# Kernel tuning notes

Hardware: AMD Instinct MI355X
Metric: run time of the kernel (lower is better)

## Reference

```python
import jax, jax.numpy as jnp
import numpy as np


def _binarize(x):
    # tf.where(x < 0, -1.0, 1.0)
    return jnp.where(x < 0, -1.0, 1.0).astype(jnp.float32)


def setup_inputs() -> dict:
    key = jax.random.key(0)
    k1, k2, k3 = jax.random.split(key, 3)
    M, K, N = 8192, 2048, 2048
    inputs = jax.random.normal(k1, (M, K), dtype=jnp.float32)
    kernel = jax.random.normal(k2, (K, N), dtype=jnp.float32) * 0.1
    bias = jax.random.normal(k3, (N,), dtype=jnp.float32) * 0.01
    return {"inputs": inputs, "kernel": kernel, "bias": bias}


def reference(inputs, kernel, bias):
    bx = _binarize(inputs)          # [M, K] in {-1, +1}
    bw = _binarize(kernel)          # [K, N] in {-1, +1}
    return jnp.matmul(bx, bw) + bias  # [M, N]
```

## Files before the change

### kernel.cpp

```cpp
#include <hip/hip_runtime.h>
#include <stdint.h>

typedef __attribute__((ext_vector_type(4))) int int4v;
typedef __attribute__((ext_vector_type(16))) unsigned char uchar16;

#define MDIM 8192
#define KDIM 2048
#define NDIM 2048
#define BM 128
#define BN 128
#define BK 128

__device__ __forceinline__ void load16_lds(const void* g, void* l) {
  __builtin_amdgcn_global_load_lds(
      (const __attribute__((address_space(1))) void*)g,
      (__attribute__((address_space(3))) void*)l, 16, 0, 0);
}

#define XBLK 4096
#define WBLK 1024

__global__ void binarize_fused(const float* __restrict__ X,
                               const float* __restrict__ W,
                               unsigned char* __restrict__ Xb,
                               unsigned char* __restrict__ WbT) {
  const int b = blockIdx.x;
  if (b < XBLK) {
    size_t i = ((size_t)b * 256 + threadIdx.x) * 16;
    const float4* xp = (const float4*)(X + i);
    uchar16 o;
#pragma unroll
    for (int h = 0; h < 4; ++h) {
      float4 a = xp[h];
      o[4 * h + 0] = (a.x < 0.f) ? 0xFFu : 0x01u;
      o[4 * h + 1] = (a.y < 0.f) ? 0xFFu : 0x01u;
      o[4 * h + 2] = (a.z < 0.f) ? 0xFFu : 0x01u;
      o[4 * h + 3] = (a.w < 0.f) ? 0xFFu : 0x01u;
    }
    *(uchar16*)(Xb + i) = o;
  } else {
    const int bw = b - XBLK;
    const int nb = bw & 31;
    const int kb = bw >> 5;
    const int nn = threadIdx.x & 63;
    const int kc = kb * 4 + (threadIdx.x >> 6);
    const float* wp = W + (size_t)(kc * 16) * NDIM + nb * 64 + nn;
    uchar16 o;
#pragma unroll
    for (int j = 0; j < 16; ++j)
      o[j] = (wp[(size_t)j * NDIM] < 0.f) ? 0xFFu : 0x01u;
    *(uchar16*)(WbT + (size_t)(nb * 64 + nn) * KDIM + kc * 16) = o;
  }
}

__global__ __launch_bounds__(256) void gemm_bin_i8(
    const unsigned char* __restrict__ A,
    const unsigned char* __restrict__ B,
    const float* __restrict__ bias,
    float* __restrict__ C) {
  __shared__ __align__(16) unsigned char As[BM * BK];
  __shared__ __align__(16) unsigned char Bs[BN * BK];

  const int tid = threadIdx.x;
  const int lane = tid & 63;
  const int wv = tid >> 6;
  const int wm = wv >> 1;
  const int wn = wv & 1;
  const int r = lane & 15;
  const int q = lane >> 4;

  const int m0 = blockIdx.x * BM;
  const int n0 = blockIdx.y * BN;

  int4v acc[4][4] = {};

  const int qbase = wv * 256;

  int srcoff[4];
#pragma unroll
  for (int i = 0; i < 4; ++i) {
    const int s = qbase + i * 64 + lane;
    const int row = s >> 3;
    const int cg = (s & 7) ^ (row & 7);
    srcoff[i] = row * KDIM + cg * 16;
  }

  for (int kb = 0; kb < KDIM; kb += BK) {
#pragma unroll
    for (int i = 0; i < 4; ++i) {
      load16_lds(A + (size_t)m0 * KDIM + kb + srcoff[i],
                 As + (size_t)(qbase + i * 64) * 16);
      load16_lds(B + (size_t)n0 * KDIM + kb + srcoff[i],
                 Bs + (size_t)(qbase + i * 64) * 16);
    }
    __syncthreads();

#pragma unroll
    for (int s2 = 0; s2 < 2; ++s2) {
      const int cswz = ((s2 * 4 + q) ^ (r & 7)) * 16;
      int4v af[4], bf[4];
#pragma unroll
      for (int t = 0; t < 4; ++t) {
        af[t] = *(const int4v*)(As + (wm * 64 + t * 16 + r) * BK + cswz);
        bf[t] = *(const int4v*)(Bs + (wn * 64 + t * 16 + r) * BK + cswz);
      }
#pragma unroll
      for (int tm = 0; tm < 4; ++tm)
#pragma unroll
        for (int tn = 0; tn < 4; ++tn)
          acc[tm][tn] = __builtin_amdgcn_mfma_i32_16x16x64_i8(
              af[tm], bf[tn], acc[tm][tn], 0, 0, 0);
    }
    __syncthreads();
  }

#pragma unroll
  for (int tn = 0; tn < 4; ++tn) {
    const int col = n0 + wn * 64 + tn * 16 + r;
    const float bv = bias[col];
#pragma unroll
    for (int tm = 0; tm < 4; ++tm) {
      const int rowb = m0 + wm * 64 + tm * 16 + q * 4;
#pragma unroll
      for (int v = 0; v < 4; ++v)
        C[(size_t)(rowb + v) * NDIM + col] = (float)acc[tm][tn][v] + bv;
    }
  }
}

extern "C" void kernel_launch(void* const* d_in, const int* in_sizes, int n_in,
                              void* d_out, int out_size, void* d_ws, size_t ws_size,
                              hipStream_t stream) {
  const float* X = (const float*)d_in[0];
  const float* W = (const float*)d_in[1];
  const float* bias = (const float*)d_in[2];
  float* out = (float*)d_out;

  unsigned char* Xb = (unsigned char*)d_ws;
  unsigned char* WbT = Xb + (size_t)MDIM * KDIM;

  binarize_fused<<<dim3(XBLK + WBLK), 256, 0, stream>>>(X, W, Xb, WbT);
  gemm_bin_i8<<<dim3(MDIM / BM, NDIM / BN), 256, 0, stream>>>(Xb, WbT, bias, out);
}
```

Baseline: 167.9 us.

## Switch binary GEMM from int8 MFMA to packed FP4 scaled MFMA

Binarized values are now packed as FP4 nibbles (±1.0 encoded as 0x2/0xA), two per byte, instead of one int8 per element. The GEMM uses the 16x16x128 f8f6f4 scaled MFMA with FP4 operand types and unit scales, halving the bytes moved per K step and doubling K per instruction. This should cut global and LDS traffic and MFMA count. The FP4 operand only fills half of each 8-int register vector, and the remaining lanes are zero-padded. Float accumulation stays exact for sums of ±1 within this range.

```diff
diff --git a/kernel.cpp b/kernel.cpp
--- a/kernel.cpp
+++ b/kernel.cpp
@@ -2,6 +2,8 @@
 #include <stdint.h>
 
 typedef __attribute__((ext_vector_type(4))) int int4v;
+typedef __attribute__((ext_vector_type(8))) int int8v;
+typedef __attribute__((ext_vector_type(4))) float floatx4;
 typedef __attribute__((ext_vector_type(16))) unsigned char uchar16;
 
 #define MDIM 8192
@@ -9,7 +11,8 @@
 #define NDIM 2048
 #define BM 128
 #define BN 128
-#define BK 128
+#define KB 1024
+#define BKB 128
 
 __device__ __forceinline__ void load16_lds(const void* g, void* l) {
   __builtin_amdgcn_global_load_lds(
@@ -17,8 +20,8 @@
       (__attribute__((address_space(3))) void*)l, 16, 0, 0);
 }
 
-#define XBLK 4096
-#define WBLK 1024
+#define XBLK 2048
+#define WBLK 512
 
 __global__ void binarize_fused(const float* __restrict__ X,
                                const float* __restrict__ W,
@@ -26,40 +29,45 @@
                                unsigned char* __restrict__ WbT) {
   const int b = blockIdx.x;
   if (b < XBLK) {
-    size_t i = ((size_t)b * 256 + threadIdx.x) * 16;
+    size_t i = ((size_t)b * 256 + threadIdx.x) * 32;
     const float4* xp = (const float4*)(X + i);
     uchar16 o;
 #pragma unroll
-    for (int h = 0; h < 4; ++h) {
+    for (int h = 0; h < 8; ++h) {
       float4 a = xp[h];
-      o[4 * h + 0] = (a.x < 0.f) ? 0xFFu : 0x01u;
-      o[4 * h + 1] = (a.y < 0.f) ? 0xFFu : 0x01u;
-      o[4 * h + 2] = (a.z < 0.f) ? 0xFFu : 0x01u;
-      o[4 * h + 3] = (a.w < 0.f) ? 0xFFu : 0x01u;
+      unsigned n0 = (a.x < 0.f) ? 0xAu : 0x2u;
+      unsigned n1 = (a.y < 0.f) ? 0xAu : 0x2u;
+      unsigned n2 = (a.z < 0.f) ? 0xAu : 0x2u;
+      unsigned n3 = (a.w < 0.f) ? 0xAu : 0x2u;
+      o[2 * h]     = (unsigned char)(n0 | (n1 << 4));
+      o[2 * h + 1] = (unsigned char)(n2 | (n3 << 4));
     }
-    *(uchar16*)(Xb + i) = o;
+    *(uchar16*)(Xb + i / 2) = o;
   } else {
     const int bw = b - XBLK;
     const int nb = bw & 31;
     const int kb = bw >> 5;
     const int nn = threadIdx.x & 63;
     const int kc = kb * 4 + (threadIdx.x >> 6);
-    const float* wp = W + (size_t)(kc * 16) * NDIM + nb * 64 + nn;
+    const float* wp = W + (size_t)(kc * 32) * NDIM + nb * 64 + nn;
     uchar16 o;
 #pragma unroll
-    for (int j = 0; j < 16; ++j)
-      o[j] = (wp[(size_t)j * NDIM] < 0.f) ? 0xFFu : 0x01u;
-    *(uchar16*)(WbT + (size_t)(nb * 64 + nn) * KDIM + kc * 16) = o;
+    for (int j = 0; j < 16; ++j) {
+      unsigned lo = (wp[(size_t)(2 * j) * NDIM] < 0.f) ? 0xAu : 0x2u;
+      unsigned hi = (wp[(size_t)(2 * j + 1) * NDIM] < 0.f) ? 0xAu : 0x2u;
+      o[j] = (unsigned char)(lo | (hi << 4));
+    }
+    *(uchar16*)(WbT + (size_t)(nb * 64 + nn) * KB + kc * 16) = o;
   }
 }
 
-__global__ __launch_bounds__(256) void gemm_bin_i8(
+__global__ __launch_bounds__(256) void gemm_bin_fp4(
     const unsigned char* __restrict__ A,
     const unsigned char* __restrict__ B,
     const float* __restrict__ bias,
     float* __restrict__ C) {
-  __shared__ __align__(16) unsigned char As[BM * BK];
-  __shared__ __align__(16) unsigned char Bs[BN * BK];
+  __shared__ __align__(16) unsigned char As[BM * BKB];
+  __shared__ __align__(16) unsigned char Bs[BN * BKB];
 
   const int tid = threadIdx.x;
   const int lane = tid & 63;
@@ -72,7 +80,7 @@
   const int m0 = blockIdx.x * BM;
   const int n0 = blockIdx.y * BN;
 
-  int4v acc[4][4] = {};
+  floatx4 acc[4][4] = {};
 
   const int qbase = wv * 256;
 
@@ -82,15 +90,15 @@
     const int s = qbase + i * 64 + lane;
     const int row = s >> 3;
     const int cg = (s & 7) ^ (row & 7);
-    srcoff[i] = row * KDIM + cg * 16;
+    srcoff[i] = row * KB + cg * 16;
   }
 
-  for (int kb = 0; kb < KDIM; kb += BK) {
+  for (int kb = 0; kb < KB; kb += BKB) {
 #pragma unroll
     for (int i = 0; i < 4; ++i) {
-      load16_lds(A + (size_t)m0 * KDIM + kb + srcoff[i],
+      load16_lds(A + (size_t)m0 * KB + kb + srcoff[i],
                  As + (size_t)(qbase + i * 64) * 16);
-      load16_lds(B + (size_t)n0 * KDIM + kb + srcoff[i],
+      load16_lds(B + (size_t)n0 * KB + kb + srcoff[i],
                  Bs + (size_t)(qbase + i * 64) * 16);
     }
     __syncthreads();
@@ -98,18 +106,21 @@
 #pragma unroll
     for (int s2 = 0; s2 < 2; ++s2) {
       const int cswz = ((s2 * 4 + q) ^ (r & 7)) * 16;
-      int4v af[4], bf[4];
+      int8v a8[4], b8[4];
 #pragma unroll
       for (int t = 0; t < 4; ++t) {
-        af[t] = *(const int4v*)(As + (wm * 64 + t * 16 + r) * BK + cswz);
-        bf[t] = *(const int4v*)(Bs + (wn * 64 + t * 16 + r) * BK + cswz);
+        int4v av = *(const int4v*)(As + (wm * 64 + t * 16 + r) * BKB + cswz);
+        int4v bv = *(const int4v*)(Bs + (wn * 64 + t * 16 + r) * BKB + cswz);
+        a8[t] = int8v{av[0], av[1], av[2], av[3], 0, 0, 0, 0};
+        b8[t] = int8v{bv[0], bv[1], bv[2], bv[3], 0, 0, 0, 0};
       }
 #pragma unroll
       for (int tm = 0; tm < 4; ++tm)
 #pragma unroll
         for (int tn = 0; tn < 4; ++tn)
-          acc[tm][tn] = __builtin_amdgcn_mfma_i32_16x16x64_i8(
-              af[tm], bf[tn], acc[tm][tn], 0, 0, 0);
+          acc[tm][tn] = __builtin_amdgcn_mfma_scale_f32_16x16x128_f8f6f4(
+              a8[tm], b8[tn], acc[tm][tn], 4, 4,
+              0, 0x7F7F7F7F, 0, 0x7F7F7F7F);
     }
     __syncthreads();
   }
@@ -123,7 +134,7 @@
       const int rowb = m0 + wm * 64 + tm * 16 + q * 4;
 #pragma unroll
       for (int v = 0; v < 4; ++v)
-        C[(size_t)(rowb + v) * NDIM + col] = (float)acc[tm][tn][v] + bv;
+        C[(size_t)(rowb + v) * NDIM + col] = acc[tm][tn][v] + bv;
     }
   }
 }
@@ -137,8 +148,8 @@
   float* out = (float*)d_out;
 
   unsigned char* Xb = (unsigned char*)d_ws;
-  unsigned char* WbT = Xb + (size_t)MDIM * KDIM;
+  unsigned char* WbT = Xb + (size_t)MDIM * KDIM / 2;
 
   binarize_fused<<<dim3(XBLK + WBLK), 256, 0, stream>>>(X, W, Xb, WbT);
-  gemm_bin_i8<<<dim3(MDIM / BM, NDIM / BN), 256, 0, stream>>>(Xb, WbT, bias, out);
+  gemm_bin_fp4<<<dim3(MDIM / BM, NDIM / BN), 256, 0, stream>>>(Xb, WbT, bias, out);
 }
```

Measured after the change: 144.7 us. -13.8%, faster.
